# Performance work log

Hardware: AMD Instinct MI355X
Metric: run time of the kernel (lower is better)

Reference implementation:

```python
import jax, jax.numpy as jnp
import numpy as np

NH, HD, MBS = 32, 64, 16   # num_heads, head_dim, mini_batch_size
BASE_LR = 1.0
ROPE_BASE = 10000.0
EPS = 1e-6


def _rotate_half(x):
    x1, x2 = jnp.split(x, 2, axis=-1)
    return jnp.concatenate((-x2, x1), axis=-1)


def _permute_qk(x):
    B, H, L, D = x.shape
    return x.reshape(B, H, L, D // 2, 2).swapaxes(-1, -2).reshape(B, H, L, D)


def _undo_permute_qk(x):
    B, H, L, D = x.shape
    return x.reshape(B, H, L, 2, D // 2).swapaxes(-1, -2).reshape(B, H, L, D)


def _ln_fwd(x, gamma, beta):
    mu = x.mean(-1, keepdims=True)
    var = x.var(-1, keepdims=True)
    return gamma * ((x - mu) / jnp.sqrt(var + EPS)) + beta


def _ln_fused_l2_bwd(x, target, gamma, beta):
    # grad of 0.5*||LN(x) - target||^2 wrt x, fused
    D = x.shape[-1]
    mu = x.mean(-1, keepdims=True)
    std = jnp.sqrt(x.var(-1, keepdims=True) + EPS)
    x_hat = (x - mu) / std
    y = gamma * x_hat + beta
    g = (y - target) * gamma
    return (D * g - g.sum(-1, keepdims=True) - x_hat * (g * x_hat).sum(-1, keepdims=True)) / (D * std)


def setup_inputs() -> dict:
    key = jax.random.key(0)
    ks = jax.random.split(key, 8)
    B, L, C, OUT = 4, 2048, 2048, 768
    s = 0.02
    return {
        "hidden_states": jax.random.normal(ks[0], (B, L, C), jnp.float32),
        "position_ids": jnp.broadcast_to(jnp.arange(L, dtype=jnp.int32)[None], (B, L)),
        "Wq": jax.random.normal(ks[1], (C, C), jnp.float32) * s,
        "Wk": jax.random.normal(ks[2], (C, C), jnp.float32) * s,
        "Wv": jax.random.normal(ks[3], (C, C), jnp.float32) * s,
        "Wo": jax.random.normal(ks[4], (C, OUT), jnp.float32) * s,
        "W1": jax.random.normal(ks[5], (NH, HD, HD), jnp.float32) * s,
        "b1": jnp.zeros((NH, 1, HD), jnp.float32),
        "ttt_lr_weight": jax.random.normal(ks[6], (NH, 1, C), jnp.float32) * s,
        "ttt_lr_bias": jnp.zeros((NH, 1), jnp.float32),
        "learnable_token_idx": jnp.zeros((MBS,), jnp.float32),
        "ttt_norm_weight": jnp.ones((NH, HD), jnp.float32),
        "ttt_norm_bias": jnp.zeros((NH, HD), jnp.float32),
        "post_norm_weight": jnp.ones((C,), jnp.float32),
        "post_norm_bias": jnp.zeros((C,), jnp.float32),
    }


def reference(hidden_states, position_ids, Wq, Wk, Wv, Wo, W1, b1,
              ttt_lr_weight, ttt_lr_bias, learnable_token_idx,
              ttt_norm_weight, ttt_norm_bias, post_norm_weight, post_norm_bias):
    B, L, C = hidden_states.shape
    NM = L // MBS
    # QKV projections -> [B, NH, L, HD]
    XQ = (hidden_states @ Wq).reshape(B, L, NH, HD).transpose(0, 2, 1, 3)
    XK = (hidden_states @ Wk).reshape(B, L, NH, HD).transpose(0, 2, 1, 3)
    XV = (hidden_states @ Wv).reshape(B, L, NH, HD).transpose(0, 2, 1, 3)
    # RoPE on positions modulo the mini-batch size
    pos = (position_ids % MBS).astype(jnp.float32)  # [B, L]
    inv_freq = 1.0 / (ROPE_BASE ** (jnp.arange(0, HD, 2, dtype=jnp.float32) / HD))
    freqs = pos[..., None] * inv_freq               # [B, L, HD/2]
    emb = jnp.concatenate((freqs, freqs), axis=-1)  # [B, L, HD]
    cos = jnp.cos(emb)[:, None]                     # [B, 1, L, HD]
    sin = jnp.sin(emb)[:, None]
    XQ, XK = _permute_qk(XQ), _permute_qk(XK)
    XQ = XQ * cos + _rotate_half(XQ) * sin
    XK = XK * cos + _rotate_half(XK) * sin
    XQ, XK = _undo_permute_qk(XQ), _undo_permute_qk(XK)
    # reshape into mini-batches: [B, NH, NM, K, HD]
    X = hidden_states.reshape(B, NM, MBS, C)
    XQ = XQ.reshape(B, NH, NM, MBS, HD)
    XK = XK.reshape(B, NH, NM, MBS, HD)
    XV = XV.reshape(B, NH, NM, MBS, HD)
    # eta: per-token learnable LR gate
    ttt_lr = jax.nn.sigmoid(
        jnp.einsum('bnkc,hdc->bhnkd', X, ttt_lr_weight)
        + ttt_lr_bias.reshape(1, NH, 1, 1, 1))              # [B,NH,NM,K,1]
    ttt_lr_eta = BASE_LR * ttt_lr.transpose(0, 1, 2, 4, 3) / HD  # [B,NH,NM,1,K]
    token_idx = jnp.clip(1.0 / jnp.arange(1, MBS + 1, dtype=jnp.float32)
                         + learnable_token_idx, 0.0, None)
    token_eta = token_idx.reshape(1, 1, 1, MBS, 1)
    eta = token_eta * ttt_lr_eta                            # [B,NH,NM,K,K]
    # TTT-Linear dual-form mini-batch scan
    ln_w = ttt_norm_weight.reshape(1, NH, 1, HD)
    ln_b = ttt_norm_bias.reshape(1, NH, 1, HD)
    W1_0 = jnp.broadcast_to(W1[None], (B, NH, HD, HD))
    b1_0 = jnp.broadcast_to(b1[None], (B, NH, 1, HD))
    tril = jnp.tril(jnp.ones((MBS, MBS), hidden_states.dtype))

    def step(carry, xs):
        W1_s, b1_s = carry
        xq, xk, xv, eta_m = xs                 # [B,NH,K,HD], eta_m [B,NH,K,K]
        Z1 = xk @ W1_s + b1_s
        target = xv - xk
        grad = _ln_fused_l2_bwd(Z1, target, ln_w, ln_b)
        Attn = tril * (xq @ xk.swapaxes(-1, -2))
        b1_bar = b1_s - (tril * eta_m) @ grad
        Z1_bar = xq @ W1_s - (eta_m * Attn) @ grad + b1_bar
        last_eta = eta_m[:, :, -1, :, None]    # [B,NH,K,1]
        W1_new = W1_s - (last_eta * xk).swapaxes(-1, -2) @ grad
        b1_new = b1_s - jnp.sum(last_eta * grad, axis=-2, keepdims=True)
        out = xq + _ln_fwd(Z1_bar, ln_w, ln_b)
        return (W1_new, b1_new), out

    xs = (XQ.transpose(2, 0, 1, 3, 4), XK.transpose(2, 0, 1, 3, 4),
          XV.transpose(2, 0, 1, 3, 4), eta.transpose(2, 0, 1, 3, 4))
    _, outs = jax.lax.scan(step, (W1_0, b1_0), xs)   # [NM,B,NH,K,HD]
    out = outs.transpose(1, 2, 0, 3, 4).reshape(B, NH, L, HD)
    out = out.transpose(0, 2, 1, 3).reshape(B, L, C)
    # post LayerNorm (eps 1e-6) and output projection
    mu = out.mean(-1, keepdims=True)
    var = out.var(-1, keepdims=True)
    out = (out - mu) / jnp.sqrt(var + EPS) * post_norm_weight + post_norm_bias
    return out @ Wo
```

## Files before the change

### kernel.cpp

```cpp
#include <hip/hip_runtime.h>
#include <cstddef>
#include <cstdint>

#define B_DIM   4
#define L_SEQ   2048
#define C_DIM   2048
#define OUT_DIM 768
#define NHEADS  32
#define HDIM    64
#define MBS_    16
#define NMINI   128
#define EPS_    1e-6f

typedef _Float16 half8 __attribute__((ext_vector_type(8)));
typedef _Float16 half4 __attribute__((ext_vector_type(4)));
typedef float floatx4 __attribute__((ext_vector_type(4)));

__device__ __forceinline__ void glds16(const void* g, void* l) {
    __builtin_amdgcn_global_load_lds(
        (const __attribute__((address_space(1))) uint32_t*)g,
        (__attribute__((address_space(3))) uint32_t*)l, 16, 0, 0);
}

__device__ __forceinline__ void split8(const float4 a, const float4 b,
                                       half8& hi, half8& lo) {
    const float x[8] = {a.x, a.y, a.z, a.w, b.x, b.y, b.z, b.w};
#pragma unroll
    for (int e = 0; e < 8; e++) {
        const _Float16 h = (_Float16)x[e];
        hi[e] = h;
        lo[e] = (_Float16)(x[e] - (float)h);
    }
}

__device__ __forceinline__ void split4(const float4 a, half4& hi, half4& lo) {
    const float x[4] = {a.x, a.y, a.z, a.w};
#pragma unroll
    for (int e = 0; e < 4; e++) {
        const _Float16 h = (_Float16)x[e];
        hi[e] = h;
        lo[e] = (_Float16)(x[e] - (float)h);
    }
}

__device__ __forceinline__ uint32_t pack_hl(float v) {
    const _Float16 h = (_Float16)v;
    const _Float16 l = (_Float16)(v - (float)h);
    union { _Float16 f[2]; uint32_t u; } p;
    p.f[0] = h; p.f[1] = l;
    return p.u;
}

__device__ __forceinline__ half8 pairswap(half8 v) {
    union { half8 h; uint32_t u[4]; } a, b;
    a.h = v;
#pragma unroll
    for (int e = 0; e < 4; e++) b.u[e] = (a.u[e] >> 16) | (a.u[e] << 16);
    return b.h;
}

template<int CTRL>
__device__ __forceinline__ float dpp_add(float v) {
    const int x = __builtin_amdgcn_update_dpp(0, __float_as_int(v), CTRL, 0xF, 0xF, false);
    return v + __int_as_float(x);
}
__device__ __forceinline__ float red16(float v) {
    v = dpp_add<0xB1>(v);
    v = dpp_add<0x4E>(v);
    v = dpp_add<0x124>(v);
    v = dpp_add<0x128>(v);
    return v;
}

__device__ __forceinline__ void bar_lgkm() {
    asm volatile("s_waitcnt lgkmcnt(0)\n\ts_barrier" ::: "memory");
}

__global__ __launch_bounds__(256)
void asplit_kernel(const float* __restrict__ A, _Float16* __restrict__ Ahi,
                   _Float16* __restrict__ Alo)
{
    const size_t idx = ((size_t)blockIdx.x * 256 + threadIdx.x) * 16;
    half8 h0, l0, h1, l1;
    {
        const float4 a = *(const float4*)(A + idx);
        const float4 b = *(const float4*)(A + idx + 4);
        split8(a, b, h0, l0);
    }
    {
        const float4 a = *(const float4*)(A + idx + 8);
        const float4 b = *(const float4*)(A + idx + 12);
        split8(a, b, h1, l1);
    }
    *(half8*)(Ahi + idx)     = h0;
    *(half8*)(Ahi + idx + 8) = h1;
    *(half8*)(Alo + idx)     = l0;
    *(half8*)(Alo + idx + 8) = l1;
}

__global__ __launch_bounds__(512)
void gemm8(const _Float16* __restrict__ Ahi, const _Float16* __restrict__ Alo,
           const _Float16* __restrict__ Bhi, const _Float16* __restrict__ Blo,
           float* __restrict__ Cout, int Ndim, int mode, int doRope)
{
    __shared__ __align__(16) _Float16 sAh[3][8192];
    __shared__ __align__(16) _Float16 sAl[3][8192];
    __shared__ __align__(16) _Float16 sBh[3][4096];
    __shared__ __align__(16) _Float16 sBl[3][4096];
    const int tid = threadIdx.x;
    const int nbx = Ndim >> 7;
    const int nwg = gridDim.x;
    int lin = blockIdx.x;
    lin = (lin & 7) * (nwg >> 3) + (lin >> 3);
    const int m0 = (lin / nbx) * 256;
    const int n0 = (lin % nbx) * 128;
    const int K = 2048;

    size_t gA[2];
    int lA[2];
#pragma unroll
    for (int X = 0; X < 2; X++) {
        const int c = X * 512 + tid;
        const int row = c >> 2, s = c & 3;
        const int ks = s ^ ((row >> 1) & 3);
        gA[X] = (size_t)(m0 + row) * K + ks * 8;
        lA[X] = c * 8;
    }
    size_t gB;
    int lB;
    {
        const int row = tid >> 2, s = tid & 3;
        const int ks = s ^ ((row >> 1) & 3);
        gB = (size_t)(n0 + row) * K + ks * 8;
        lB = tid * 8;
    }

    const int lane = tid & 63, q = lane >> 4, lc = lane & 15;
    const int w = tid >> 6, wm = w >> 1, wn = w & 1;
    int offA[4], offB[4];
#pragma unroll
    for (int i = 0; i < 4; i++) {
        const int rA = wm * 64 + i * 16 + lc;
        offA[i] = rA * 32 + ((q ^ ((rA >> 1) & 3)) << 3);
    }
#pragma unroll
    for (int j = 0; j < 4; j++) {
        const int rB = wn * 64 + j * 16 + lc;
        offB[j] = rB * 32 + ((q ^ ((rB >> 1) & 3)) << 3);
    }

    floatx4 acc[4][4];
#pragma unroll
    for (int i = 0; i < 4; i++)
#pragma unroll
        for (int j = 0; j < 4; j++) acc[i][j] = (floatx4)0.0f;

#define STAGE(T)                                                         \
    {                                                                    \
        const int b_ = (T) % 3;                                          \
        const int ko_ = (T) * 32;                                        \
        glds16(Ahi + gA[0] + ko_, &sAh[b_][lA[0]]);                      \
        glds16(Alo + gA[0] + ko_, &sAl[b_][lA[0]]);                      \
        glds16(Ahi + gA[1] + ko_, &sAh[b_][lA[1]]);                      \
        glds16(Alo + gA[1] + ko_, &sAl[b_][lA[1]]);                      \
        glds16(Bhi + gB + ko_,    &sBh[b_][lB]);                         \
        glds16(Blo + gB + ko_,    &sBl[b_][lB]);                         \
    }

#define FRAGS(B_)                                                        \
    half8 ah[4], al[4], bh[4], bl[4];                                    \
    _Pragma("unroll")                                                    \
    for (int i = 0; i < 4; i++) {                                        \
        ah[i] = *(const half8*)&sAh[B_][offA[i]];                        \
        al[i] = *(const half8*)&sAl[B_][offA[i]];                        \
    }                                                                    \
    _Pragma("unroll")                                                    \
    for (int j = 0; j < 4; j++) {                                        \
        bh[j] = *(const half8*)&sBh[B_][offB[j]];                        \
        bl[j] = *(const half8*)&sBl[B_][offB[j]];                        \
    }

#define MFMAS                                                            \
    __builtin_amdgcn_s_setprio(1);                                       \
    _Pragma("unroll")                                                    \
    for (int i = 0; i < 4; i++)                                          \
        _Pragma("unroll")                                                \
        for (int j = 0; j < 4; j++) {                                    \
            acc[i][j] = __builtin_amdgcn_mfma_f32_16x16x32_f16(ah[i], bh[j], acc[i][j], 0, 0, 0); \
            acc[i][j] = __builtin_amdgcn_mfma_f32_16x16x32_f16(ah[i], bl[j], acc[i][j], 0, 0, 0); \
            acc[i][j] = __builtin_amdgcn_mfma_f32_16x16x32_f16(al[i], bh[j], acc[i][j], 0, 0, 0); \
        }                                                                \
    __builtin_amdgcn_s_setprio(0);

    STAGE(0)
    STAGE(1)
    asm volatile("s_waitcnt vmcnt(6) lgkmcnt(0)\n\ts_barrier" ::: "memory");

    for (int t = 0; t < 62; t++) {
        const int b = t % 3;
        FRAGS(b)
        STAGE(t + 2)
        MFMAS
        asm volatile("s_waitcnt vmcnt(6) lgkmcnt(0)\n\ts_barrier" ::: "memory");
    }
    {
        FRAGS(2)
        MFMAS
        asm volatile("s_waitcnt vmcnt(0) lgkmcnt(0)\n\ts_barrier" ::: "memory");
    }
    {
        FRAGS(0)
        MFMAS
    }
#undef STAGE
#undef FRAGS
#undef MFMAS

    float cs[4][4], sn[4][4];
    if (doRope) {
#pragma unroll
        for (int j = 0; j < 4; j++) {
            const int ii = ((j * 16 + lc) & 63) >> 1;
            const float invf = expf(-(float)ii * 0.28782313662425574f);
#pragma unroll
            for (int r = 0; r < 4; r++) {
                const float ang = (float)(q * 4 + r) * invf;
                sincosf(ang, &sn[j][r], &cs[j][r]);
            }
        }
    }
    const int oddcol = lc & 1;
#pragma unroll
    for (int i = 0; i < 4; i++) {
#pragma unroll
        for (int j = 0; j < 4; j++) {
            floatx4 v = acc[i][j];
            if (doRope) {
#pragma unroll
                for (int r = 0; r < 4; r++) {
                    const float partner = __shfl_xor(v[r], 1);
                    v[r] = v[r] * cs[j][r] + partner * (oddcol ? sn[j][r] : -sn[j][r]);
                }
            }
            const int n = n0 + wn * 64 + j * 16 + lc;
            if (mode == 0) {
                const int h = (n >> 6) & 31, d = n & 63;
#pragma unroll
                for (int r = 0; r < 4; r++) {
                    const int m = m0 + wm * 64 + i * 16 + q * 4 + r;
                    const int b = m >> 11, li = m & 2047;
                    Cout[((size_t)(b * 32 + h) * 2048 + li) * 64 + d] = v[r];
                }
            } else {
#pragma unroll
                for (int r = 0; r < 4; r++) {
                    const int m = m0 + wm * 64 + i * 16 + q * 4 + r;
                    Cout[(size_t)m * OUT_DIM + n] = v[r];
                }
            }
        }
    }
}

__global__ __launch_bounds__(256)
void gemm_f32(const float* __restrict__ A,
              const _Float16* __restrict__ Bhi, const _Float16* __restrict__ Blo,
              float* __restrict__ Cout, int mode, int doRope)
{
    __shared__ __align__(16) float    sA[4096];
    __shared__ __align__(16) _Float16 sBhi[4096];
    __shared__ __align__(16) _Float16 sBlo[4096];
    const int tid = threadIdx.x;
    const int m0 = blockIdx.y * 128, n0 = blockIdx.x * 128;
    const int K = 2048;

    size_t gA[4]; float* lA[4];
#pragma unroll
    for (int I = 0; I < 4; I++) {
        const int c = I * 256 + tid;
        const int row = c >> 3, seg = (c & 7) ^ (row & 7);
        gA[I] = (size_t)(m0 + row) * K + seg * 4;
        lA[I] = &sA[c * 4];
    }
    size_t gB[2]; _Float16 *lBh[2], *lBl[2];
#pragma unroll
    for (int I = 0; I < 2; I++) {
        const int c = I * 256 + tid;
        const int row = c >> 2, seg = (c & 3) ^ ((row >> 1) & 3);
        gB[I] = (size_t)(n0 + row) * K + seg * 8;
        lBh[I] = &sBhi[c * 8];
        lBl[I] = &sBlo[c * 8];
    }

    const int lane = tid & 63, quad = lane >> 4, lc = lane & 15;
    const int wv = tid >> 6, wm = wv & 1, wn = wv >> 1;
    int offA0[4], offA1[4], offB[4];
#pragma unroll
    for (int i = 0; i < 4; i++) {
        const int rA = wm * 64 + i * 16 + lc;
        offA0[i] = (rA * 8 + ((2 * quad)     ^ (rA & 7))) * 4;
        offA1[i] = (rA * 8 + ((2 * quad + 1) ^ (rA & 7))) * 4;
    }
#pragma unroll
    for (int j = 0; j < 4; j++) {
        const int rB = wn * 64 + j * 16 + lc;
        offB[j] = (rB * 4 + (quad ^ ((rB >> 1) & 3))) * 8;
    }

    floatx4 acc[4][4];
#pragma unroll
    for (int i = 0; i < 4; i++)
#pragma unroll
        for (int j = 0; j < 4; j++) acc[i][j] = (floatx4)0.0f;

    for (int k0 = 0; k0 < K; k0 += 32) {
        __syncthreads();
#pragma unroll
        for (int I = 0; I < 4; I++) glds16(A + gA[I] + k0, lA[I]);
#pragma unroll
        for (int I = 0; I < 2; I++) {
            glds16(Bhi + gB[I] + k0, lBh[I]);
            glds16(Blo + gB[I] + k0, lBl[I]);
        }
        __syncthreads();

        half8 ah[4], al[4], bh[4], bl[4];
#pragma unroll
        for (int i = 0; i < 4; i++) {
            const float4 va = *(const float4*)&sA[offA0[i]];
            const float4 vb = *(const float4*)&sA[offA1[i]];
            split8(va, vb, ah[i], al[i]);
        }
#pragma unroll
        for (int j = 0; j < 4; j++) {
            bh[j] = *(const half8*)&sBhi[offB[j]];
            bl[j] = *(const half8*)&sBlo[offB[j]];
        }
#pragma unroll
        for (int i = 0; i < 4; i++)
#pragma unroll
            for (int j = 0; j < 4; j++) {
                acc[i][j] = __builtin_amdgcn_mfma_f32_16x16x32_f16(ah[i], bh[j], acc[i][j], 0, 0, 0);
                acc[i][j] = __builtin_amdgcn_mfma_f32_16x16x32_f16(ah[i], bl[j], acc[i][j], 0, 0, 0);
                acc[i][j] = __builtin_amdgcn_mfma_f32_16x16x32_f16(al[i], bh[j], acc[i][j], 0, 0, 0);
            }
    }

    float cs[4][4], sn[4][4];
    if (doRope) {
#pragma unroll
        for (int j = 0; j < 4; j++) {
            const int ii = ((j * 16 + lc) & 63) >> 1;
            const float invf = expf(-(float)ii * 0.28782313662425574f);
#pragma unroll
            for (int r = 0; r < 4; r++) {
                const float ang = (float)(quad * 4 + r) * invf;
                sincosf(ang, &sn[j][r], &cs[j][r]);
            }
        }
    }
    const int oddcol = lc & 1;
#pragma unroll
    for (int i = 0; i < 4; i++) {
#pragma unroll
        for (int j = 0; j < 4; j++) {
            floatx4 v = acc[i][j];
            if (doRope) {
#pragma unroll
                for (int r = 0; r < 4; r++) {
                    const float partner = __shfl_xor(v[r], 1);
                    v[r] = v[r] * cs[j][r] + partner * (oddcol ? sn[j][r] : -sn[j][r]);
                }
            }
            const int n = n0 + wn * 64 + j * 16 + lc;
            if (mode == 0) {
                const int h = (n >> 6) & 31, d = n & 63;
#pragma unroll
                for (int r = 0; r < 4; r++) {
                    const int m = m0 + wm * 64 + i * 16 + quad * 4 + r;
                    const int b = m >> 11, li = m & 2047;
                    Cout[((size_t)(b * 32 + h) * 2048 + li) * 64 + d] = v[r];
                }
            } else {
#pragma unroll
                for (int r = 0; r < 4; r++) {
                    const int m = m0 + wm * 64 + i * 16 + quad * 4 + r;
                    Cout[(size_t)m * OUT_DIM + n] = v[r];
                }
            }
        }
    }
}

__global__ __launch_bounds__(256)
void wtrans_kernel(const float* __restrict__ W, _Float16* __restrict__ BThi,
                   _Float16* __restrict__ BTlo, int Nw)
{
    __shared__ float tile[32][33];
    const int t = threadIdx.x, tx = t & 31, ty = t >> 5;
    const int n0 = blockIdx.x * 32, k0 = blockIdx.y * 32;
    const int K = 2048;
#pragma unroll
    for (int r = 0; r < 4; r++)
        tile[ty + r * 8][tx] = W[(size_t)(k0 + ty + r * 8) * Nw + n0 + tx];
    __syncthreads();
#pragma unroll
    for (int r = 0; r < 4; r++) {
        const float val = tile[tx][ty + r * 8];
        const _Float16 hh = (_Float16)val;
        const size_t o = (size_t)(n0 + ty + r * 8) * K + k0 + tx;
        BThi[o] = hh;
        BTlo[o] = (_Float16)(val - (float)hh);
    }
}

__global__ __launch_bounds__(256)
void lr_kernel(const float* __restrict__ hidden, const float* __restrict__ wlr,
               const float* __restrict__ lr_bias, float* __restrict__ lrs)
{
    __shared__ float sRow[2048];
    __shared__ float sPart[32][9];
    const int m = blockIdx.x;
    const int t = threadIdx.x;
    const float* row = hidden + (size_t)m * C_DIM;
#pragma unroll
    for (int j = 0; j < 8; j++) sRow[t + j * 256] = row[t + j * 256];
    __syncthreads();
    const int h = t >> 3, p = t & 7;
    const float* w = wlr + (size_t)h * C_DIM;
    float s = 0.0f;
#pragma unroll 8
    for (int k = 0; k < 64; k++) {
        const int c = k * 32 + p * 4;
        const float4 a = *(const float4*)(sRow + c);
        const float4 b = *(const float4*)(w + c);
        s += a.x * b.x + a.y * b.y + a.z * b.z + a.w * b.w;
    }
    sPart[h][p] = s;
    __syncthreads();
    if (t < 32) {
        float v = 0.0f;
#pragma unroll
        for (int p2 = 0; p2 < 8; p2++) v += sPart[t][p2];
        v += lr_bias[t];
        const float sig = 1.0f / (1.0f + expf(-v));
        lrs[((size_t)(m >> 11) * NHEADS + t) * L_SEQ + (m & 2047)] = sig;
    }
}

__global__ __launch_bounds__(256, 1)
void scan_mfma(const float* __restrict__ XQ, const float* __restrict__ XK,
               float* __restrict__ XVo, const float* __restrict__ LRS,
               const float* __restrict__ W1i, const float* __restrict__ b1i,
               const float* __restrict__ lt, const float* __restrict__ lnw,
               const float* __restrict__ lnb)
{
    __shared__ __align__(16) _Float16 sXqH[1024], sXqL[1024];
    __shared__ __align__(16) _Float16 sXkH[1024], sXkL[1024];
    __shared__ __align__(16) float    sTgt[16 * 68];
    __shared__ __align__(16) float    sXq32[2][16 * 68];
    __shared__ __align__(16) _Float16 sW1H[4096], sW1L[4096];
    __shared__ __align__(16) uint32_t sKT[64 * 20];
    __shared__ __align__(16) uint32_t sCf[16 * 20];
    __shared__ __align__(16) float sRedA[16 * 36];
    __shared__ __align__(16) float sRedC[16 * 12];
    __shared__ __align__(16) float sEta[16];
    __shared__ float sB1[64];

    const int bh = blockIdx.x, h = bh & 31;
    const int t = threadIdx.x;
    const int lane = t & 63, q = lane >> 4, lc = lane & 15;
    const int w = t >> 6;
    const int col = w * 16 + lc;
    const int iRow = t >> 4;
    const int m = t & 15;

    if (t < 64) sB1[t] = b1i[h * 64 + t];

    float w1s[4][4];
#pragma unroll
    for (int t4 = 0; t4 < 4; t4++)
#pragma unroll
        for (int r = 0; r < 4; r++) {
            const float v = W1i[h * 4096 + (16 * t4 + lc) * 64 + (16 * w + 4 * q + r)];
            w1s[t4][r] = v;
            const int nn = 16 * w + 4 * q + r, k = 16 * t4 + lc;
            const int off = nn * 64 + ((((k >> 3) ^ (nn & 7)) << 3) | (k & 7));
            const _Float16 hh = (_Float16)v;
            sW1H[off] = hh; sW1L[off] = (_Float16)(v - (float)hh);
        }

    const float gamC = lnw[h * 64 + col], betC = lnb[h * 64 + col];
    const float g2c = gamC * gamC;
    float sumG2 = 0.0f;
#pragma unroll
    for (int d0 = 0; d0 < 16; d0++) {
        const float4 gv = *(const float4*)(lnw + h * 64 + d0 * 4);
        sumG2 += gv.x * gv.x + gv.y * gv.y + gv.z * gv.z + gv.w * gv.w;
    }
    float tokR[4];
#pragma unroll
    for (int r = 0; r < 4; r++)
        tokR[r] = fmaxf(1.0f / (float)(4 * q + r + 1) + lt[4 * q + r], 0.0f);
    const float tok15 = fmaxf(1.0f / 16.0f + lt[15], 0.0f);

    __syncthreads();

    const size_t base = (size_t)bh * L_SEQ * HDIM;
    const float* xq_g = XQ + base;
    const float* xk_g = XK + base;
    float* xv_g = XVo + base;
    const float* lr_g = LRS + (size_t)bh * L_SEQ;

    float4 cq = *(const float4*)(xq_g + t * 4);
    float4 ck = *(const float4*)(xk_g + t * 4);
    float4 cv = *(const float4*)(xv_g + t * 4);
    float clr = lr_g[m];

    const int rw = 16 * w + lc;
    const int stOff = iRow * 64 + ((((m >> 1) ^ (iRow & 7)) << 3) | ((m & 1) << 2));
    const int gkm = (m ^ (m >> 2)) & 3;
    const int ktWb = 4 * (w ^ gkm) + q;

    for (int n = 0; n < NMINI; n++) {
        const int buf = n & 1;
        {
            half4 hq, lq, hk, lk;
            split4(cq, hq, lq);
            split4(ck, hk, lk);
            *(half4*)&sXqH[stOff] = hq;
            *(half4*)&sXqL[stOff] = lq;
            *(half4*)&sXkH[stOff] = hk;
            *(half4*)&sXkL[stOff] = lk;
            const float4 tg = make_float4(cv.x - ck.x, cv.y - ck.y,
                                          cv.z - ck.z, cv.w - ck.w);
            *(float4*)&sTgt[iRow * 68 + m * 4] = tg;
            *(float4*)&sXq32[buf][iRow * 68 + m * 4] = cq;
            const float kvv[4] = {ck.x, ck.y, ck.z, ck.w};
#pragma unroll
            for (int i2 = 0; i2 < 4; i2++)
                sKT[(4 * m + i2) * 20 + ktWb] = pack_hl(kvv[i2]);
        }
        if (t < 16) sEta[t] = clr * (1.0f / 64.0f);
        const int np = (n + 1) & (NMINI - 1);
        const float4 nq = *(const float4*)(xq_g + np * 1024 + t * 4);
        const float4 nk = *(const float4*)(xk_g + np * 1024 + t * 4);
        const float4 nv = *(const float4*)(xv_g + np * 1024 + t * 4);
        const float nlr = lr_g[np * 16 + m];
        bar_lgkm();

        const float b1c = sB1[col];
        const float4 ev = *(const float4*)&sEta[4 * q];
        const float evv[4] = {ev.x, ev.y, ev.z, ev.w};

        half8 qh[2], ql[2], kh[2], kl[2], wh[2], wl[2];
#pragma unroll
        for (int f = 0; f < 2; f++) {
            const int cx = ((4 * f + q) ^ (lc & 7)) << 3;
            qh[f] = *(const half8*)&sXqH[lc * 64 + cx];
            ql[f] = *(const half8*)&sXqL[lc * 64 + cx];
            kh[f] = *(const half8*)&sXkH[lc * 64 + cx];
            kl[f] = *(const half8*)&sXkL[lc * 64 + cx];
            const int cw = ((4 * f + q) ^ (rw & 7)) << 3;
            wh[f] = *(const half8*)&sW1H[rw * 64 + cw];
            wl[f] = *(const half8*)&sW1L[rw * 64 + cw];
        }

        floatx4 z1a = (floatx4)0.0f, zba = (floatx4)0.0f, at = (floatx4)0.0f;
#pragma unroll
        for (int f = 0; f < 2; f++) {
            z1a = __builtin_amdgcn_mfma_f32_16x16x32_f16(kh[f], wh[f], z1a, 0, 0, 0);
            z1a = __builtin_amdgcn_mfma_f32_16x16x32_f16(kh[f], wl[f], z1a, 0, 0, 0);
            z1a = __builtin_amdgcn_mfma_f32_16x16x32_f16(kl[f], wh[f], z1a, 0, 0, 0);
            zba = __builtin_amdgcn_mfma_f32_16x16x32_f16(qh[f], wh[f], zba, 0, 0, 0);
            zba = __builtin_amdgcn_mfma_f32_16x16x32_f16(qh[f], wl[f], zba, 0, 0, 0);
            zba = __builtin_amdgcn_mfma_f32_16x16x32_f16(ql[f], wh[f], zba, 0, 0, 0);
        }
        if (w == 0) {
            const float etaLC = sEta[lc];
#pragma unroll
            for (int f = 0; f < 2; f++) {
                at = __builtin_amdgcn_mfma_f32_16x16x32_f16(qh[f], kh[f], at, 0, 0, 0);
                at = __builtin_amdgcn_mfma_f32_16x16x32_f16(qh[f], kl[f], at, 0, 0, 0);
                at = __builtin_amdgcn_mfma_f32_16x16x32_f16(ql[f], kh[f], at, 0, 0, 0);
            }
#pragma unroll
            for (int r = 0; r < 4; r++) {
                const int i = 4 * q + r;
                const float cfv = (lc <= i) ? -tokR[r] * etaLC * (at[r] + 1.0f) : 0.0f;
                sCf[i * 20 + 4 * ((lc >> 2) ^ q) + (lc & 3)] = pack_hl(cfv);
            }
        }

        float z[4], cE[4];
        float sz[4], szz[4], sgz[4], sgzz[4], sc[4], scz[4];
#pragma unroll
        for (int r = 0; r < 4; r++) {
            const int row = 4 * q + r;
            z[r] = z1a[r] + b1c;
            const float tgt = sTgt[row * 68 + col];
            cE[r] = gamC * (betC - tgt);
            const float zz = z[r] * z[r];
            sz[r]   = red16(z[r]);
            szz[r]  = red16(zz);
            sgz[r]  = red16(g2c * z[r]);
            sgzz[r] = red16(g2c * zz);
            sc[r]   = red16(cE[r]);
            scz[r]  = red16(cE[r] * z[r]);
        }
        if (lc == 0) {
#pragma unroll
            for (int r = 0; r < 4; r++) {
                const int rb = (4 * q + r) * 36;
                sRedA[rb + 0  + w] = sz[r];
                sRedA[rb + 4  + w] = szz[r];
                sRedA[rb + 8  + w] = sgz[r];
                sRedA[rb + 12 + w] = sgzz[r];
                sRedA[rb + 16 + w] = sc[r];
                sRedA[rb + 20 + w] = scz[r];
            }
        }
        bar_lgkm();

        half8 ktp[4];
#pragma unroll
        for (int t4 = 0; t4 < 4; t4++) {
            const int gkr = ((lc >> 2) ^ t4) & 3;
            ktp[t4] = *(const half8*)&sKT[(16 * t4 + lc) * 20 + 4 * (q ^ gkr)];
        }
        const half8 cfp = *(const half8*)&sCf[lc * 20 + 4 * (q ^ (lc >> 2))];

        float gr[4];
#pragma unroll
        for (int r = 0; r < 4; r++) {
            const int rb = (4 * q + r) * 36;
            const float4 a0 = *(const float4*)&sRedA[rb + 0];
            const float4 a1 = *(const float4*)&sRedA[rb + 4];
            const float4 a2 = *(const float4*)&sRedA[rb + 8];
            const float4 a3 = *(const float4*)&sRedA[rb + 12];
            const float4 a4 = *(const float4*)&sRedA[rb + 16];
            const float4 a5 = *(const float4*)&sRedA[rb + 20];
            const float Sz   = a0.x + a0.y + a0.z + a0.w;
            const float Szz  = a1.x + a1.y + a1.z + a1.w;
            const float Sgz  = a2.x + a2.y + a2.z + a2.w;
            const float Sgzz = a3.x + a3.y + a3.z + a3.w;
            const float Sc   = a4.x + a4.y + a4.z + a4.w;
            const float Scz  = a5.x + a5.y + a5.z + a5.w;
            const float mu  = Sz * (1.0f / 64.0f);
            const float ex2 = Szz * (1.0f / 64.0f);
            const float rs  = rsqrtf(ex2 - mu * mu + EPS_);
            const float G1 = rs * (Sgz - mu * sumG2) + Sc;
            const float G2 = rs * rs * (Sgzz - 2.0f * mu * Sgz + mu * mu * sumG2)
                           + rs * (Scz - mu * Sc);
            const float xh = (z[r] - mu) * rs;
            const float g  = g2c * xh + cE[r];
            gr[r] = (64.0f * g - G1 - xh * G2) * rs * (1.0f / 64.0f);
        }

        half8 gf, gfl;
#pragma unroll
        for (int r = 0; r < 4; r++) {
            const _Float16 h0 = (_Float16)gr[r];
            gf[2 * r]     = h0;
            gf[2 * r + 1] = (_Float16)(gr[r] - (float)h0);
            const float gl = gr[r] * (tok15 * evv[r]);
            const _Float16 h1 = (_Float16)gl;
            gfl[2 * r]     = h1;
            gfl[2 * r + 1] = (_Float16)(gl - (float)h1);
        }
        const half8 gfs  = pairswap(gf);
        const half8 gfls = pairswap(gfl);

        zba = __builtin_amdgcn_mfma_f32_16x16x32_f16(cfp, gf,  zba, 0, 0, 0);
        zba = __builtin_amdgcn_mfma_f32_16x16x32_f16(cfp, gfs, zba, 0, 0, 0);
#pragma unroll
        for (int t4 = 0; t4 < 4; t4++) {
            floatx4 up = (floatx4)0.0f;
            up = __builtin_amdgcn_mfma_f32_16x16x32_f16(gfl,  ktp[t4], up, 0, 0, 0);
            up = __builtin_amdgcn_mfma_f32_16x16x32_f16(gfls, ktp[t4], up, 0, 0, 0);
#pragma unroll
            for (int r = 0; r < 4; r++) w1s[t4][r] -= up[r];
        }

        float z2[4], p1[4], p2[4];
#pragma unroll
        for (int r = 0; r < 4; r++) {
            z2[r] = zba[r] + b1c;
            p1[r] = red16(z2[r]);
            p2[r] = red16(z2[r] * z2[r]);
        }
        if (lc == 0)
#pragma unroll
            for (int r = 0; r < 4; r++) {
                const int rb = (4 * q + r) * 12;
                sRedC[rb + w]     = p1[r];
                sRedC[rb + 4 + w] = p2[r];
            }

        {
            float p = gr[0] * evv[0] + gr[1] * evv[1] + gr[2] * evv[2] + gr[3] * evv[3];
            p += __shfl_xor(p, 16);
            p += __shfl_xor(p, 32);
            if (q == 0) sB1[col] -= tok15 * p;
        }
#pragma unroll
        for (int t4 = 0; t4 < 4; t4++)
#pragma unroll
            for (int r = 0; r < 4; r++) {
                const int nn = 16 * w + 4 * q + r, k = 16 * t4 + lc;
                const int off = nn * 64 + ((((k >> 3) ^ (nn & 7)) << 3) | (k & 7));
                const float v = w1s[t4][r];
                const _Float16 hh = (_Float16)v;
                sW1H[off] = hh; sW1L[off] = (_Float16)(v - (float)hh);
            }
        bar_lgkm();

#pragma unroll
        for (int r = 0; r < 4; r++) {
            const int row = 4 * q + r;
            const float4 a = *(const float4*)&sRedC[row * 12];
            const float4 b = *(const float4*)&sRedC[row * 12 + 4];
            const float mu  = (a.x + a.y + a.z + a.w) * (1.0f / 64.0f);
            const float ex2 = (b.x + b.y + b.z + b.w) * (1.0f / 64.0f);
            const float rs  = rsqrtf(ex2 - mu * mu + EPS_);
            const float xqv = sXq32[buf][row * 68 + col];
            xv_g[n * 1024 + row * 64 + col] = xqv + gamC * ((z2[r] - mu) * rs) + betC;
        }
        cq = nq; ck = nk; cv = nv; clr = nlr;
    }
}

__global__ __launch_bounds__(256)
void postln_kernel(const float* __restrict__ Ob, const float* __restrict__ pnw,
                   const float* __restrict__ pnb, _Float16* __restrict__ XNhi,
                   _Float16* __restrict__ XNlo)
{
    const int m = blockIdx.x;
    const int b = m >> 11, l = m & 2047;
    const int t = threadIdx.x;
    float v[8];
    float s1 = 0.0f, s2 = 0.0f;
    const int c0 = t * 8;
    const int hh = c0 >> 6, d0 = c0 & 63;
    const float* bas = Ob + (size_t)b * NHEADS * L_SEQ * HDIM + (size_t)l * HDIM
                     + (size_t)hh * (L_SEQ * HDIM) + d0;
    {
        const float4 va = *(const float4*)(bas);
        const float4 vb = *(const float4*)(bas + 4);
        v[0] = va.x; v[1] = va.y; v[2] = va.z; v[3] = va.w;
        v[4] = vb.x; v[5] = vb.y; v[6] = vb.z; v[7] = vb.w;
    }
#pragma unroll
    for (int j = 0; j < 8; j++) { s1 += v[j]; s2 += v[j] * v[j]; }
#pragma unroll
    for (int o = 1; o < 64; o <<= 1) { s1 += __shfl_xor(s1, o); s2 += __shfl_xor(s2, o); }
    __shared__ float r1[4], r2[4];
    const int w = t >> 6;
    if ((t & 63) == 0) { r1[w] = s1; r2[w] = s2; }
    __syncthreads();
    s1 = r1[0] + r1[1] + r1[2] + r1[3];
    s2 = r2[0] + r2[1] + r2[2] + r2[3];
    const float mu = s1 * (1.0f / 2048.0f);
    const float var = s2 * (1.0f / 2048.0f) - mu * mu;
    const float rstd = rsqrtf(var + EPS_);
    half8 oh, ol;
#pragma unroll
    for (int j = 0; j < 8; j++) {
        const float y = (v[j] - mu) * rstd * pnw[c0 + j] + pnb[c0 + j];
        const _Float16 hy = (_Float16)y;
        oh[j] = hy;
        ol[j] = (_Float16)(y - (float)hy);
    }
    *(half8*)(XNhi + (size_t)m * C_DIM + c0) = oh;
    *(half8*)(XNlo + (size_t)m * C_DIM + c0) = ol;
}

extern "C" void kernel_launch(void* const* d_in, const int* in_sizes, int n_in,
                              void* d_out, int out_size, void* d_ws, size_t ws_size,
                              hipStream_t stream)
{
    (void)in_sizes; (void)n_in; (void)out_size;
    const float* hidden  = (const float*)d_in[0];
    const float* Wq      = (const float*)d_in[2];
    const float* Wk      = (const float*)d_in[3];
    const float* Wv      = (const float*)d_in[4];
    const float* Wo      = (const float*)d_in[5];
    const float* W1      = (const float*)d_in[6];
    const float* b1      = (const float*)d_in[7];
    const float* wlr     = (const float*)d_in[8];
    const float* lr_bias = (const float*)d_in[9];
    const float* lt      = (const float*)d_in[10];
    const float* lnw     = (const float*)d_in[11];
    const float* lnb     = (const float*)d_in[12];
    const float* pnw     = (const float*)d_in[13];
    const float* pnb     = (const float*)d_in[14];

    const size_t TEN = (size_t)B_DIM * NHEADS * L_SEQ * HDIM;
    float* XQ  = (float*)d_ws;
    float* XK  = XQ + TEN;
    float* XVo = XK + TEN;
    float* LRS = XVo + TEN;
    _Float16* Ahi = (_Float16*)(LRS + 262144);
    _Float16* Alo = Ahi + TEN;
    const size_t needBytes = (3 * TEN + 262144) * 4 + TEN * 4;
    const int useAsplit = (ws_size >= needBytes) ? 1 : 0;
    const dim3 blk(256);

    _Float16* BThi = (_Float16*)d_out;
    _Float16* BTlo = BThi + (size_t)C_DIM * C_DIM;

    lr_kernel<<<dim3(B_DIM * L_SEQ), blk, 0, stream>>>(hidden, wlr, lr_bias, LRS);
    if (useAsplit)
        asplit_kernel<<<dim3(4096), blk, 0, stream>>>(hidden, Ahi, Alo);

    const float* Wmats[3] = {Wq, Wk, Wv};
    float* outs[3] = {XQ, XK, XVo};
    for (int p = 0; p < 3; p++) {
        wtrans_kernel<<<dim3(64, 64), blk, 0, stream>>>(Wmats[p], BThi, BTlo, C_DIM);
        if (useAsplit)
            gemm8<<<dim3(512), dim3(512), 0, stream>>>(Ahi, Alo, BThi, BTlo,
                                                       outs[p], C_DIM,
                                                       0, (p < 2) ? 1 : 0);
        else
            gemm_f32<<<dim3(16, 64), blk, 0, stream>>>(hidden, BThi, BTlo,
                                                       outs[p], 0, (p < 2) ? 1 : 0);
    }
    scan_mfma<<<dim3(B_DIM * NHEADS), blk, 0, stream>>>(XQ, XK, XVo, LRS,
                                                        W1, b1, lt, lnw, lnb);
    _Float16* XNhi = (_Float16*)XQ;
    _Float16* XNlo = XNhi + TEN;
    _Float16* WThi = (_Float16*)XK;
    _Float16* WTlo = WThi + (size_t)OUT_DIM * C_DIM;
    postln_kernel<<<dim3(B_DIM * L_SEQ), blk, 0, stream>>>(XVo, pnw, pnb,
                                                           XNhi, XNlo);
    wtrans_kernel<<<dim3(24, 64), blk, 0, stream>>>(Wo, WThi, WTlo, OUT_DIM);
    gemm8<<<dim3(192), dim3(512), 0, stream>>>(XNhi, XNlo, WThi, WTlo,
                                               (float*)d_out, OUT_DIM, 1, 0);
}
```

Baseline: 1.402 ms.

## Fuse QKV projections into one GEMM and pipeline scan output epilogue

Merges the three Q/K/V projection GEMMs into a single launch over a concatenated transposed weight (N=6144), with all four weight transposes/splits done in one kernel and the fp16 hi/lo split of hidden states folded into the lr kernel. In the scan, the per-minibatch output LayerNorm store is deferred into the next iteration after the first barrier, removing one barrier per step. It double-buffers the K-transpose tile and splits MFMA accumulator chains to expose more ILP. The fused path needs a larger workspace and falls back to the old per-projection sequence otherwise.

After: 1.396 ms. No clear change (-0.4%).

```diff
diff --git a/kernel.cpp b/kernel.cpp
--- a/kernel.cpp
+++ b/kernel.cpp
@@ -74,28 +74,6 @@
 
 __device__ __forceinline__ void bar_lgkm() {
     asm volatile("s_waitcnt lgkmcnt(0)\n\ts_barrier" ::: "memory");
-}
-
-__global__ __launch_bounds__(256)
-void asplit_kernel(const float* __restrict__ A, _Float16* __restrict__ Ahi,
-                   _Float16* __restrict__ Alo)
-{
-    const size_t idx = ((size_t)blockIdx.x * 256 + threadIdx.x) * 16;
-    half8 h0, l0, h1, l1;
-    {
-        const float4 a = *(const float4*)(A + idx);
-        const float4 b = *(const float4*)(A + idx + 4);
-        split8(a, b, h0, l0);
-    }
-    {
-        const float4 a = *(const float4*)(A + idx + 8);
-        const float4 b = *(const float4*)(A + idx + 12);
-        split8(a, b, h1, l1);
-    }
-    *(half8*)(Ahi + idx)     = h0;
-    *(half8*)(Ahi + idx + 8) = h1;
-    *(half8*)(Alo + idx)     = l0;
-    *(half8*)(Alo + idx + 8) = l1;
 }
 
 __global__ __launch_bounds__(512)
@@ -235,21 +213,23 @@
 #pragma unroll
         for (int j = 0; j < 4; j++) {
             floatx4 v = acc[i][j];
-            if (doRope) {
+            const int n = n0 + wn * 64 + j * 16 + lc;
+            if (doRope && n < 4096) {
 #pragma unroll
                 for (int r = 0; r < 4; r++) {
                     const float partner = __shfl_xor(v[r], 1);
                     v[r] = v[r] * cs[j][r] + partner * (oddcol ? sn[j][r] : -sn[j][r]);
                 }
             }
-            const int n = n0 + wn * 64 + j * 16 + lc;
             if (mode == 0) {
+                const int p = n >> 11;
                 const int h = (n >> 6) & 31, d = n & 63;
 #pragma unroll
                 for (int r = 0; r < 4; r++) {
                     const int m = m0 + wm * 64 + i * 16 + q * 4 + r;
                     const int b = m >> 11, li = m & 2047;
-                    Cout[((size_t)(b * 32 + h) * 2048 + li) * 64 + d] = v[r];
+                    Cout[(size_t)p * 16777216 +
+                         ((size_t)(b * 32 + h) * 2048 + li) * 64 + d] = v[r];
                 }
             } else {
 #pragma unroll
@@ -415,8 +395,50 @@
 }
 
 __global__ __launch_bounds__(256)
+void wtrans_all(const float* __restrict__ Wq, const float* __restrict__ Wk,
+                const float* __restrict__ Wv, const float* __restrict__ Wo,
+                _Float16* __restrict__ BThi, _Float16* __restrict__ BTlo,
+                _Float16* __restrict__ WThi, _Float16* __restrict__ WTlo)
+{
+    __shared__ float tile[32][33];
+    const int t = threadIdx.x, tx = t & 31, ty = t >> 5;
+    const int id = blockIdx.x;
+    const float* W;
+    _Float16 *dh, *dl;
+    int Nw, bx, by;
+    if (id < 12288) {
+        const int p = id >> 12;
+        const int r = id & 4095;
+        bx = r & 63; by = r >> 6;
+        W = (p == 0) ? Wq : (p == 1) ? Wk : Wv;
+        dh = BThi + (size_t)p * C_DIM * C_DIM;
+        dl = BTlo + (size_t)p * C_DIM * C_DIM;
+        Nw = C_DIM;
+    } else {
+        const int r = id - 12288;
+        bx = r % 24; by = r / 24;
+        W = Wo; dh = WThi; dl = WTlo; Nw = OUT_DIM;
+    }
+    const int n0 = bx * 32, k0 = by * 32;
+    const int K = 2048;
+#pragma unroll
+    for (int r = 0; r < 4; r++)
+        tile[ty + r * 8][tx] = W[(size_t)(k0 + ty + r * 8) * Nw + n0 + tx];
+    __syncthreads();
+#pragma unroll
+    for (int r = 0; r < 4; r++) {
+        const float val = tile[tx][ty + r * 8];
+        const _Float16 hh = (_Float16)val;
+        const size_t o = (size_t)(n0 + ty + r * 8) * K + k0 + tx;
+        dh[o] = hh;
+        dl[o] = (_Float16)(val - (float)hh);
+    }
+}
+
+__global__ __launch_bounds__(256)
 void lr_kernel(const float* __restrict__ hidden, const float* __restrict__ wlr,
-               const float* __restrict__ lr_bias, float* __restrict__ lrs)
+               const float* __restrict__ lr_bias, float* __restrict__ lrs,
+               _Float16* __restrict__ Ahi, _Float16* __restrict__ Alo)
 {
     __shared__ float sRow[2048];
     __shared__ float sPart[32][9];
@@ -426,6 +448,14 @@
 #pragma unroll
     for (int j = 0; j < 8; j++) sRow[t + j * 256] = row[t + j * 256];
     __syncthreads();
+    if (Ahi) {
+        const float4 a = *(const float4*)(sRow + t * 8);
+        const float4 b = *(const float4*)(sRow + t * 8 + 4);
+        half8 hh, ll;
+        split8(a, b, hh, ll);
+        *(half8*)(Ahi + (size_t)m * C_DIM + t * 8) = hh;
+        *(half8*)(Alo + (size_t)m * C_DIM + t * 8) = ll;
+    }
     const int h = t >> 3, p = t & 7;
     const float* w = wlr + (size_t)h * C_DIM;
     float s = 0.0f;
@@ -460,7 +490,7 @@
     __shared__ __align__(16) float    sTgt[16 * 68];
     __shared__ __align__(16) float    sXq32[2][16 * 68];
     __shared__ __align__(16) _Float16 sW1H[4096], sW1L[4096];
-    __shared__ __align__(16) uint32_t sKT[64 * 20];
+    __shared__ __align__(16) uint32_t sKT[2][64 * 20];
     __shared__ __align__(16) uint32_t sCf[16 * 20];
     __shared__ __align__(16) float sRedA[16 * 36];
     __shared__ __align__(16) float sRedC[16 * 12];
@@ -522,8 +552,15 @@
     const int gkm = (m ^ (m >> 2)) & 3;
     const int ktWb = 4 * (w ^ gkm) + q;
 
+    float z2p[4] = {0.0f, 0.0f, 0.0f, 0.0f};
+
     for (int n = 0; n < NMINI; n++) {
         const int buf = n & 1;
+        const int np = (n + 1) & (NMINI - 1);
+        const float4 nq = *(const float4*)(xq_g + np * 1024 + t * 4);
+        const float4 nk = *(const float4*)(xk_g + np * 1024 + t * 4);
+        const float4 nv = *(const float4*)(xv_g + np * 1024 + t * 4);
+        const float nlr = lr_g[np * 16 + m];
         {
             half4 hq, lq, hk, lk;
             split4(cq, hq, lq);
@@ -539,15 +576,26 @@
             const float kvv[4] = {ck.x, ck.y, ck.z, ck.w};
 #pragma unroll
             for (int i2 = 0; i2 < 4; i2++)
-                sKT[(4 * m + i2) * 20 + ktWb] = pack_hl(kvv[i2]);
+                sKT[buf][(4 * m + i2) * 20 + ktWb] = pack_hl(kvv[i2]);
         }
         if (t < 16) sEta[t] = clr * (1.0f / 64.0f);
-        const int np = (n + 1) & (NMINI - 1);
-        const float4 nq = *(const float4*)(xq_g + np * 1024 + t * 4);
-        const float4 nk = *(const float4*)(xk_g + np * 1024 + t * 4);
-        const float4 nv = *(const float4*)(xv_g + np * 1024 + t * 4);
-        const float nlr = lr_g[np * 16 + m];
         bar_lgkm();
+
+        if (n) {
+            const int pb = buf ^ 1;
+#pragma unroll
+            for (int r = 0; r < 4; r++) {
+                const int row = 4 * q + r;
+                const float4 a = *(const float4*)&sRedC[row * 12];
+                const float4 b = *(const float4*)&sRedC[row * 12 + 4];
+                const float mu  = (a.x + a.y + a.z + a.w) * (1.0f / 64.0f);
+                const float ex2 = (b.x + b.y + b.z + b.w) * (1.0f / 64.0f);
+                const float rs  = rsqrtf(ex2 - mu * mu + EPS_);
+                const float xqv = sXq32[pb][row * 68 + col];
+                xv_g[(n - 1) * 1024 + row * 64 + col] =
+                    xqv + gamC * ((z2p[r] - mu) * rs) + betC;
+            }
+        }
 
         const float b1c = sB1[col];
         const float4 ev = *(const float4*)&sEta[4 * q];
@@ -566,28 +614,34 @@
             wl[f] = *(const half8*)&sW1L[rw * 64 + cw];
         }
 
-        floatx4 z1a = (floatx4)0.0f, zba = (floatx4)0.0f, at = (floatx4)0.0f;
-#pragma unroll
-        for (int f = 0; f < 2; f++) {
-            z1a = __builtin_amdgcn_mfma_f32_16x16x32_f16(kh[f], wh[f], z1a, 0, 0, 0);
-            z1a = __builtin_amdgcn_mfma_f32_16x16x32_f16(kh[f], wl[f], z1a, 0, 0, 0);
-            z1a = __builtin_amdgcn_mfma_f32_16x16x32_f16(kl[f], wh[f], z1a, 0, 0, 0);
-            zba = __builtin_amdgcn_mfma_f32_16x16x32_f16(qh[f], wh[f], zba, 0, 0, 0);
-            zba = __builtin_amdgcn_mfma_f32_16x16x32_f16(qh[f], wl[f], zba, 0, 0, 0);
-            zba = __builtin_amdgcn_mfma_f32_16x16x32_f16(ql[f], wh[f], zba, 0, 0, 0);
-        }
+        floatx4 z1a = (floatx4)0.0f, z1b = (floatx4)0.0f;
+        floatx4 zb0 = (floatx4)0.0f, zb1 = (floatx4)0.0f;
+        z1a = __builtin_amdgcn_mfma_f32_16x16x32_f16(kh[0], wh[0], z1a, 0, 0, 0);
+        z1a = __builtin_amdgcn_mfma_f32_16x16x32_f16(kh[0], wl[0], z1a, 0, 0, 0);
+        z1a = __builtin_amdgcn_mfma_f32_16x16x32_f16(kl[0], wh[0], z1a, 0, 0, 0);
+        z1b = __builtin_amdgcn_mfma_f32_16x16x32_f16(kh[1], wh[1], z1b, 0, 0, 0);
+        z1b = __builtin_amdgcn_mfma_f32_16x16x32_f16(kh[1], wl[1], z1b, 0, 0, 0);
+        z1b = __builtin_amdgcn_mfma_f32_16x16x32_f16(kl[1], wh[1], z1b, 0, 0, 0);
+        zb0 = __builtin_amdgcn_mfma_f32_16x16x32_f16(qh[0], wh[0], zb0, 0, 0, 0);
+        zb0 = __builtin_amdgcn_mfma_f32_16x16x32_f16(qh[0], wl[0], zb0, 0, 0, 0);
+        zb0 = __builtin_amdgcn_mfma_f32_16x16x32_f16(ql[0], wh[0], zb0, 0, 0, 0);
+        zb1 = __builtin_amdgcn_mfma_f32_16x16x32_f16(qh[1], wh[1], zb1, 0, 0, 0);
+        zb1 = __builtin_amdgcn_mfma_f32_16x16x32_f16(qh[1], wl[1], zb1, 0, 0, 0);
+        zb1 = __builtin_amdgcn_mfma_f32_16x16x32_f16(ql[1], wh[1], zb1, 0, 0, 0);
         if (w == 0) {
             const float etaLC = sEta[lc];
-#pragma unroll
-            for (int f = 0; f < 2; f++) {
-                at = __builtin_amdgcn_mfma_f32_16x16x32_f16(qh[f], kh[f], at, 0, 0, 0);
-                at = __builtin_amdgcn_mfma_f32_16x16x32_f16(qh[f], kl[f], at, 0, 0, 0);
-                at = __builtin_amdgcn_mfma_f32_16x16x32_f16(ql[f], kh[f], at, 0, 0, 0);
-            }
+            floatx4 at0 = (floatx4)0.0f, at1 = (floatx4)0.0f;
+            at0 = __builtin_amdgcn_mfma_f32_16x16x32_f16(qh[0], kh[0], at0, 0, 0, 0);
+            at0 = __builtin_amdgcn_mfma_f32_16x16x32_f16(qh[0], kl[0], at0, 0, 0, 0);
+            at0 = __builtin_amdgcn_mfma_f32_16x16x32_f16(ql[0], kh[0], at0, 0, 0, 0);
+            at1 = __builtin_amdgcn_mfma_f32_16x16x32_f16(qh[1], kh[1], at1, 0, 0, 0);
+            at1 = __builtin_amdgcn_mfma_f32_16x16x32_f16(qh[1], kl[1], at1, 0, 0, 0);
+            at1 = __builtin_amdgcn_mfma_f32_16x16x32_f16(ql[1], kh[1], at1, 0, 0, 0);
 #pragma unroll
             for (int r = 0; r < 4; r++) {
                 const int i = 4 * q + r;
-                const float cfv = (lc <= i) ? -tokR[r] * etaLC * (at[r] + 1.0f) : 0.0f;
+                const float atv = at0[r] + at1[r];
+                const float cfv = (lc <= i) ? -tokR[r] * etaLC * (atv + 1.0f) : 0.0f;
                 sCf[i * 20 + 4 * ((lc >> 2) ^ q) + (lc & 3)] = pack_hl(cfv);
             }
         }
@@ -597,7 +651,7 @@
 #pragma unroll
         for (int r = 0; r < 4; r++) {
             const int row = 4 * q + r;
-            z[r] = z1a[r] + b1c;
+            z[r] = z1a[r] + z1b[r] + b1c;
             const float tgt = sTgt[row * 68 + col];
             cE[r] = gamC * (betC - tgt);
             const float zz = z[r] * z[r];
@@ -626,7 +680,7 @@
 #pragma unroll
         for (int t4 = 0; t4 < 4; t4++) {
             const int gkr = ((lc >> 2) ^ t4) & 3;
-            ktp[t4] = *(const half8*)&sKT[(16 * t4 + lc) * 20 + 4 * (q ^ gkr)];
+            ktp[t4] = *(const half8*)&sKT[buf][(16 * t4 + lc) * 20 + 4 * (q ^ gkr)];
         }
         const half8 cfp = *(const half8*)&sCf[lc * 20 + 4 * (q ^ (lc >> 2))];
 
@@ -671,6 +725,9 @@
         const half8 gfs  = pairswap(gf);
         const half8 gfls = pairswap(gfl);
 
+        floatx4 zba;
+#pragma unroll
+        for (int r = 0; r < 4; r++) zba[r] = zb0[r] + zb1[r];
         zba = __builtin_amdgcn_mfma_f32_16x16x32_f16(cfp, gf,  zba, 0, 0, 0);
         zba = __builtin_amdgcn_mfma_f32_16x16x32_f16(cfp, gfs, zba, 0, 0, 0);
 #pragma unroll
@@ -713,20 +770,24 @@
                 const _Float16 hh = (_Float16)v;
                 sW1H[off] = hh; sW1L[off] = (_Float16)(v - (float)hh);
             }
-        bar_lgkm();
-
-#pragma unroll
-        for (int r = 0; r < 4; r++) {
-            const int row = 4 * q + r;
-            const float4 a = *(const float4*)&sRedC[row * 12];
-            const float4 b = *(const float4*)&sRedC[row * 12 + 4];
-            const float mu  = (a.x + a.y + a.z + a.w) * (1.0f / 64.0f);
-            const float ex2 = (b.x + b.y + b.z + b.w) * (1.0f / 64.0f);
-            const float rs  = rsqrtf(ex2 - mu * mu + EPS_);
-            const float xqv = sXq32[buf][row * 68 + col];
-            xv_g[n * 1024 + row * 64 + col] = xqv + gamC * ((z2[r] - mu) * rs) + betC;
-        }
+
+#pragma unroll
+        for (int r = 0; r < 4; r++) z2p[r] = z2[r];
         cq = nq; ck = nk; cv = nv; clr = nlr;
+    }
+
+    bar_lgkm();
+#pragma unroll
+    for (int r = 0; r < 4; r++) {
+        const int row = 4 * q + r;
+        const float4 a = *(const float4*)&sRedC[row * 12];
+        const float4 b = *(const float4*)&sRedC[row * 12 + 4];
+        const float mu  = (a.x + a.y + a.z + a.w) * (1.0f / 64.0f);
+        const float ex2 = (b.x + b.y + b.z + b.w) * (1.0f / 64.0f);
+        const float rs  = rsqrtf(ex2 - mu * mu + EPS_);
+        const float xqv = sXq32[1][row * 68 + col];
+        xv_g[(NMINI - 1) * 1024 + row * 64 + col] =
+            xqv + gamC * ((z2p[r] - mu) * rs) + betC;
     }
 }
 
@@ -802,38 +863,55 @@
     float* LRS = XVo + TEN;
     _Float16* Ahi = (_Float16*)(LRS + 262144);
     _Float16* Alo = Ahi + TEN;
-    const size_t needBytes = (3 * TEN + 262144) * 4 + TEN * 4;
-    const int useAsplit = (ws_size >= needBytes) ? 1 : 0;
+    _Float16* BThi = Alo + TEN;
+    _Float16* BTlo = BThi + 3 * (size_t)C_DIM * C_DIM;
+    _Float16* WThi = BTlo + 3 * (size_t)C_DIM * C_DIM;
+    _Float16* WTlo = WThi + (size_t)OUT_DIM * C_DIM;
+    const size_t needBytes =
+        (3 * TEN + 262144) * 4
+        + TEN * 2 * 2
+        + 3 * (size_t)C_DIM * C_DIM * 4
+        + (size_t)OUT_DIM * C_DIM * 4;
+    const int fused = (ws_size >= needBytes) ? 1 : 0;
     const dim3 blk(256);
 
-    _Float16* BThi = (_Float16*)d_out;
-    _Float16* BTlo = BThi + (size_t)C_DIM * C_DIM;
-
-    lr_kernel<<<dim3(B_DIM * L_SEQ), blk, 0, stream>>>(hidden, wlr, lr_bias, LRS);
-    if (useAsplit)
-        asplit_kernel<<<dim3(4096), blk, 0, stream>>>(hidden, Ahi, Alo);
-
-    const float* Wmats[3] = {Wq, Wk, Wv};
-    float* outs[3] = {XQ, XK, XVo};
-    for (int p = 0; p < 3; p++) {
-        wtrans_kernel<<<dim3(64, 64), blk, 0, stream>>>(Wmats[p], BThi, BTlo, C_DIM);
-        if (useAsplit)
-            gemm8<<<dim3(512), dim3(512), 0, stream>>>(Ahi, Alo, BThi, BTlo,
-                                                       outs[p], C_DIM,
-                                                       0, (p < 2) ? 1 : 0);
-        else
-            gemm_f32<<<dim3(16, 64), blk, 0, stream>>>(hidden, BThi, BTlo,
+    if (fused) {
+        lr_kernel<<<dim3(B_DIM * L_SEQ), blk, 0, stream>>>(hidden, wlr, lr_bias,
+                                                           LRS, Ahi, Alo);
+        wtrans_all<<<dim3(13824), blk, 0, stream>>>(Wq, Wk, Wv, Wo,
+                                                    BThi, BTlo, WThi, WTlo);
+        gemm8<<<dim3(1536), dim3(512), 0, stream>>>(Ahi, Alo, BThi, BTlo,
+                                                    XQ, 3 * C_DIM, 0, 1);
+        scan_mfma<<<dim3(B_DIM * NHEADS), blk, 0, stream>>>(XQ, XK, XVo, LRS,
+                                                            W1, b1, lt, lnw, lnb);
+        _Float16* XNhi = (_Float16*)XQ;
+        _Float16* XNlo = XNhi + TEN;
+        postln_kernel<<<dim3(B_DIM * L_SEQ), blk, 0, stream>>>(XVo, pnw, pnb,
+                                                               XNhi, XNlo);
+        gemm8<<<dim3(192), dim3(512), 0, stream>>>(XNhi, XNlo, WThi, WTlo,
+                                                   (float*)d_out, OUT_DIM, 1, 0);
+    } else {
+        _Float16* FBhi = (_Float16*)d_out;
+        _Float16* FBlo = FBhi + (size_t)C_DIM * C_DIM;
+        lr_kernel<<<dim3(B_DIM * L_SEQ), blk, 0, stream>>>(hidden, wlr, lr_bias,
+                                                           LRS, nullptr, nullptr);
+        const float* Wmats[3] = {Wq, Wk, Wv};
+        float* outs[3] = {XQ, XK, XVo};
+        for (int p = 0; p < 3; p++) {
+            wtrans_kernel<<<dim3(64, 64), blk, 0, stream>>>(Wmats[p], FBhi, FBlo, C_DIM);
+            gemm_f32<<<dim3(16, 64), blk, 0, stream>>>(hidden, FBhi, FBlo,
                                                        outs[p], 0, (p < 2) ? 1 : 0);
-    }
-    scan_mfma<<<dim3(B_DIM * NHEADS), blk, 0, stream>>>(XQ, XK, XVo, LRS,
-                                                        W1, b1, lt, lnw, lnb);
-    _Float16* XNhi = (_Float16*)XQ;
-    _Float16* XNlo = XNhi + TEN;
-    _Float16* WThi = (_Float16*)XK;
-    _Float16* WTlo = WThi + (size_t)OUT_DIM * C_DIM;
-    postln_kernel<<<dim3(B_DIM * L_SEQ), blk, 0, stream>>>(XVo, pnw, pnb,
-                                                           XNhi, XNlo);
-    wtrans_kernel<<<dim3(24, 64), blk, 0, stream>>>(Wo, WThi, WTlo, OUT_DIM);
-    gemm8<<<dim3(192), dim3(512), 0, stream>>>(XNhi, XNlo, WThi, WTlo,
-                                               (float*)d_out, OUT_DIM, 1, 0);
-}
+        }
+        scan_mfma<<<dim3(B_DIM * NHEADS), blk, 0, stream>>>(XQ, XK, XVo, LRS,
+                                                            W1, b1, lt, lnw, lnb);
+        _Float16* XNhi = (_Float16*)XQ;
+        _Float16* XNlo = XNhi + TEN;
+        _Float16* FWhi = (_Float16*)XK;
+        _Float16* FWlo = FWhi + (size_t)OUT_DIM * C_DIM;
+        postln_kernel<<<dim3(B_DIM * L_SEQ), blk, 0, stream>>>(XVo, pnw, pnb,
+                                                               XNhi, XNlo);
+        wtrans_kernel<<<dim3(24, 64), blk, 0, stream>>>(Wo, FWhi, FWlo, OUT_DIM);
+        gemm8<<<dim3(192), dim3(512), 0, stream>>>(XNhi, XNlo, FWhi, FWlo,
+                                                   (float*)d_out, OUT_DIM, 1, 0);
+    }
+}
```
